# Performance work log

Measured on AMD Instinct MI355X. Metric: run time of the kernel, lower is better.

## Reference

```python
import jax, jax.numpy as jnp
import numpy as np
from jax import lax

B, LATENT, HC, COND_OUT, H, INPUT = 64, 512, 1024, 512, 1024, 389
S, SEQ = 16, 512
NOTES = SEQ // S  # 32 notes per subsequence
NL = 2


def _lstm_cell(x, h, c, Wih, Whh, bih, bhh):
    # PyTorch LSTM cell, gate order i, f, g, o
    g = x @ Wih.T + h @ Whh.T + bih + bhh
    i, f, gg, o = jnp.split(g, 4, axis=-1)
    c_new = jax.nn.sigmoid(f) * c + jax.nn.sigmoid(i) * jnp.tanh(gg)
    h_new = jax.nn.sigmoid(o) * jnp.tanh(c_new)
    return h_new, c_new


def setup_inputs() -> dict:
    key = jax.random.key(0)
    ks = iter(jax.random.split(key, 32))
    s = 0.03  # ~ PyTorch LSTM uniform(-1/sqrt(H), 1/sqrt(H)) scale
    def W(shape):
        return jax.random.normal(next(ks), shape, jnp.float32) * s
    return {
        "latent": jax.random.normal(next(ks), (B, LATENT), jnp.float32),
        "target": jax.random.randint(next(ks), (B, SEQ), 0, INPUT),
        "teacher_forcing": 0,
        "h0_dec": jax.random.normal(next(ks), (S, NL, B, H), jnp.float32),
        "c0_dec": jax.random.normal(next(ks), (S, NL, B, H), jnp.float32),
        # conductor LSTM (2 layers)
        "Wih_c0": W((4 * HC, LATENT)), "Whh_c0": W((4 * HC, HC)),
        "bih_c0": W((4 * HC,)), "bhh_c0": W((4 * HC,)),
        "Wih_c1": W((4 * HC, HC)), "Whh_c1": W((4 * HC, HC)),
        "bih_c1": W((4 * HC,)), "bhh_c1": W((4 * HC,)),
        # conductor output projection
        "Wco": W((COND_OUT, HC)), "bco": W((COND_OUT,)),
        # decoder LSTM (2 layers); input = concat(prev_note, emb) -> INPUT+COND_OUT
        "Wih_d0": W((4 * H, INPUT + COND_OUT)), "Whh_d0": W((4 * H, H)),
        "bih_d0": W((4 * H,)), "bhh_d0": W((4 * H,)),
        "Wih_d1": W((4 * H, H)), "Whh_d1": W((4 * H, H)),
        "bih_d1": W((4 * H,)), "bhh_d1": W((4 * H,)),
        # decoder output projection
        "Wdo": W((INPUT, H)), "bdo": W((INPUT,)),
    }


def reference(latent, target, teacher_forcing, h0_dec, c0_dec,
              Wih_c0, Whh_c0, bih_c0, bhh_c0, Wih_c1, Whh_c1, bih_c1, bhh_c1,
              Wco, bco,
              Wih_d0, Whh_d0, bih_d0, bhh_d0, Wih_d1, Whh_d1, bih_d1, bhh_d1,
              Wdo, bdo):
    # use_teacher_forcing is hard-coded False in the source; target is unused.
    del target, teacher_forcing

    def outer(carry, xs):
        hc, cc, prev = carry          # hc, cc: [2,B,HC]; prev: [B,INPUT]
        hd_init, cd_init = xs         # [2,B,H] random decoder init per subsequence
        h0, c0 = _lstm_cell(latent, hc[0], cc[0], Wih_c0, Whh_c0, bih_c0, bhh_c0)
        h1, c1 = _lstm_cell(h0, hc[1], cc[1], Wih_c1, Whh_c1, bih_c1, bhh_c1)
        emb = jnp.tanh(h1 @ Wco.T + bco)  # [B, COND_OUT]

        def inner(ic, _):
            p, hdi, cdi = ic
            x = jnp.concatenate([p, emb], axis=-1)  # [B, INPUT+COND_OUT]
            hd0, cd0 = _lstm_cell(x, hdi[0], cdi[0], Wih_d0, Whh_d0, bih_d0, bhh_d0)
            hd1, cd1 = _lstm_cell(hd0, hdi[1], cdi[1], Wih_d1, Whh_d1, bih_d1, bhh_d1)
            note = jnp.tanh(hd1 @ Wdo.T + bdo)  # [B, INPUT]
            return (note, jnp.stack([hd0, hd1]), jnp.stack([cd0, cd1])), note

        (prev_new, _, _), notes = lax.scan(inner, (prev, hd_init, cd_init), None, length=NOTES)
        return (jnp.stack([h0, h1]), jnp.stack([c0, c1]), prev_new), notes

    init = (jnp.zeros((NL, B, HC), jnp.float32),
            jnp.zeros((NL, B, HC), jnp.float32),
            jnp.zeros((B, INPUT), jnp.float32))
    _, out = lax.scan(outer, init, (h0_dec, c0_dec))
    # out: [S, NOTES, B, INPUT] -> [B, SEQ, INPUT]
    return out.transpose(2, 0, 1, 3).reshape(B, SEQ, INPUT)
```

## Files before the change

### kernel.cpp

```cpp
#include <hip/hip_runtime.h>
#include <hip/hip_bf16.h>

typedef unsigned int  u32;
typedef unsigned short u16;
typedef __attribute__((ext_vector_type(8))) short short8;
typedef __attribute__((ext_vector_type(4))) float f32x4;
typedef __attribute__((ext_vector_type(4))) unsigned int u32x4;
typedef __attribute__((ext_vector_type(2))) unsigned int u32x2;

#define MFMA(a,b,c) __builtin_amdgcn_mfma_f32_16x16x32_bf16(a,b,c,0,0,0)

#define NWG    256
#define KD0    1448
#define KD1    2056
#define KPROJ  1032

#define WS_ARR   0
#define WS_DONE  1024

#define WS_NOTE  4096
#define WS_HD0   (WS_NOTE + 2*52*64*8*2)
#define WS_HD1   (WS_HD0 + 2*128*64*8*2)
#define WS_HC0   (WS_HD1 + 2*128*64*8*2)
#define WS_HC1   (WS_HC0 + 2*128*64*8*2)
#define WS_EMB   (WS_HC1 + 2*128*64*8*2)
#define WS_LAT   (WS_EMB + 15*64*64*8*2)
#define WS_END   (WS_EMB + 16*64*64*8*2)

#define NOTE_PAR 26624
#define HD_PAR   65536
#define HC_PAR   65536
#define EMB_S    32768

#define L_GSC   0
#define L_GC0X  8448
#define L_CC0   12800
#define L_CC1   13824
#define L_BC1   14848
#define L_PACK  14912
#define L_ROLE  16960
#define L_WD0   L_ROLE
#define L_G0E   (L_ROLE + 32*KD0*2)
#define L_CST0  (L_G0E + 8448)
#define L_BD0   (L_CST0 + 2048)
#define L_WPJ   (L_BD0 + 128)
#define L_BPJ   (L_WPJ + 16*KPROJ*2)
#define L_WD1   L_ROLE
#define L_CST1  (L_ROLE + 32*KD1*2)
#define L_BD1   (L_CST1 + 2048)
#define LDS_BYTES 153600

__device__ __forceinline__ u16 f2bf(float f){
  u32 u = __float_as_uint(f);
  u32 r = (u + 0x7FFFu + ((u >> 16) & 1u)) >> 16;
  return (u16)r;
}
__device__ __forceinline__ float sigm(float x){ return 1.f/(1.f + __expf(-x)); }
__device__ __forceinline__ float tanh_(float x){
  float e = __expf(-2.f*fabsf(x));
  float t = (1.f - e)/(1.f + e);
  return x < 0.f ? -t : t;
}
__device__ __forceinline__ short8 ldw8(const float* p0){
  short8 r;
#pragma unroll
  for (int j = 0; j < 8; ++j) r[j] = (short)f2bf(p0[j]);
  return r;
}

__device__ __forceinline__ void gst1(u32* p, u32 v){
  asm volatile("global_store_dword %0, %1, off sc1" :: "v"(p), "v"(v) : "memory");
}
__device__ __forceinline__ void gst4(u16* p, u32x4 v){
  asm volatile("global_store_dwordx4 %0, %1, off sc1" :: "v"(p), "v"(v) : "memory");
}
__device__ __forceinline__ u32 ld1_sc1(const u32* p){
  u32 v;
  asm volatile("global_load_dword %0, %1, off sc1\n\ts_waitcnt vmcnt(0)"
               : "=v"(v) : "v"(p) : "memory");
  return v;
}

#define AISSUE(dst, addr) \
  asm volatile("global_load_dwordx4 %0, %1, off sc1" : "=&v"(dst) : "v"(addr) : "memory")
#define AWAITN(cnt) do{ \
  asm volatile("s_waitcnt vmcnt(" #cnt ")" ::: "memory"); \
  __builtin_amdgcn_sched_barrier(0x3F7); }while(0)

template<int NA, int NB, bool TWO>
__device__ __forceinline__ void mm_lds(
    const u16* Wl, int ldw16, const u16* xal, const u16* xbl,
    f32x4& a0, f32x4& a1)
{
  constexpr int N = NA + NB;
  short8 ab[(N < 16) ? N : 16];
#define XADDR(i) (((i) < NA) ? (xal + (size_t)(i)*2048) : (xbl + (size_t)((i)-NA)*2048))
#define ACONS(i) { \
    a0 = MFMA(ab[(i)&15], *(const short8*)(Wl + (size_t)(i)*32), a0); \
    if constexpr (TWO) a1 = MFMA(ab[(i)&15], *(const short8*)(Wl + ldw16 + (size_t)(i)*32), a1); }
  if constexpr (N <= 16){
#pragma unroll
    for (int i = 0; i < N; ++i) AISSUE(ab[i], XADDR(i));
    AWAITN(0);
#pragma unroll
    for (int i = 0; i < N; ++i) ACONS(i);
  } else {
#pragma unroll
    for (int i = 0; i < 16; ++i) AISSUE(ab[i], XADDR(i));
#pragma unroll
    for (int i = 0; i < N - 16; ++i){
      AWAITN(15);
      ACONS(i);
      AISSUE(ab[i & 15], XADDR(i + 16));
    }
#define ATAIL(j, c) AWAITN(c); ACONS(N - 16 + (j));
    ATAIL(0,15) ATAIL(1,14) ATAIL(2,13) ATAIL(3,12)
    ATAIL(4,11) ATAIL(5,10) ATAIL(6,9)  ATAIL(7,8)
    ATAIL(8,7)  ATAIL(9,6)  ATAIL(10,5) ATAIL(11,4)
    ATAIL(12,3) ATAIL(13,2) ATAIL(14,1) ATAIL(15,0)
#undef ATAIL
  }
#undef ACONS
#undef XADDR
}

template<int NA, int NB, bool TWO>
__device__ __forceinline__ void mm_gw(
    const float* w00, const float* w01, const float* w10, const float* w11,
    const u16* xal, const u16* xbl, f32x4& a0, f32x4& a1)
{
  constexpr int N = NA + NB;
  static_assert((N % 16) == 0, "");
  short8 ab[16];
#define XADDR(i) (((i) < NA) ? (xal + (size_t)(i)*2048) : (xbl + (size_t)((i)-NA)*2048))
#pragma unroll
  for (int b = 0; b < N/16; ++b){
#pragma unroll
    for (int j = 0; j < 16; ++j) AISSUE(ab[j], XADDR(b*16 + j));
    AWAITN(0);
#pragma unroll
    for (int j = 0; j < 16; ++j){
      const int i = b*16 + j;
      const float* wp0 = (i < NA) ? (w00 + (size_t)i*32) : (w01 + (size_t)(i-NA)*32);
      a0 = MFMA(ab[j], ldw8(wp0), a0);
      if constexpr (TWO){
        const float* wp1 = (i < NA) ? (w10 + (size_t)i*32) : (w11 + (size_t)(i-NA)*32);
        a1 = MFMA(ab[j], ldw8(wp1), a1);
      }
    }
  }
#undef XADDR
}

__device__ __forceinline__ void gbar(char* ws, int grp, int mem, u32 ep){
  u32* arr  = (u32*)(ws + WS_ARR) + grp*32;
  u32* done = (u32*)(ws + WS_DONE);
  asm volatile("s_waitcnt vmcnt(0)" ::: "memory");
  __syncthreads();
  if (threadIdx.x < 64){
    const int l = threadIdx.x;
    if (l == 0) gst1(&arr[mem], ep);
    if (mem == 0){
      for (;;){
        u32 m = (l < 32) ? ld1_sc1(&arr[l]) : ep;
#pragma unroll
        for (int off = 32; off; off >>= 1){
          u32 o = (u32)__shfl_xor((int)m, off, 64);
          m = o < m ? o : m;
        }
        if (m >= ep) break;
      }
      if (l == 0) gst1(&done[grp], ep);
    }
    for (;;){
      u32 m = (l < 8) ? ld1_sc1(&done[l]) : ep;
#pragma unroll
      for (int off = 32; off; off >>= 1){
        u32 o = (u32)__shfl_xor((int)m, off, 64);
        m = o < m ? o : m;
      }
      if (m >= ep) break;
      __builtin_amdgcn_s_sleep(1);
    }
  }
  __syncthreads();
}

struct Params {
  const float *latent, *h0_dec, *c0_dec;
  const float *Wih_c0, *Whh_c0, *bih_c0, *bhh_c0;
  const float *Wih_c1, *Whh_c1, *bih_c1, *bhh_c1;
  const float *Wco, *bco;
  const float *Wih_d0, *Whh_d0, *bih_d0, *bhh_d0;
  const float *Wih_d1, *Whh_d1, *bih_d1, *bhh_d1;
  const float *Wdo, *bdo;
  float* out;
  char* ws;
};

__device__ __forceinline__ void cell_pw(
    const float* g_sc, const float* gadd, const float* bias,
    float* cst, u32* pack, int tid)
{
  const int b = tid & 63, k = tid >> 6;
  u32 hp = 0;
#pragma unroll
  for (int j = 0; j < 2; ++j){
    const int u = 2*k + j;
    float gi = g_sc[b*33 + u];
    float gf = g_sc[b*33 + 8 + u];
    float gg = g_sc[b*33 + 16 + u];
    float go = g_sc[b*33 + 24 + u];
    if (gadd){
      gi += gadd[b*33 + u];      gf += gadd[b*33 + 8 + u];
      gg += gadd[b*33 + 16 + u]; go += gadd[b*33 + 24 + u];
    }
    if (bias){
      gi += bias[u]; gf += bias[8 + u]; gg += bias[16 + u]; go += bias[24 + u];
    }
    float c = sigm(gf)*cst[u*64 + b] + sigm(gi)*tanh_(gg);
    const float h = sigm(go)*tanh_(c);
    cst[u*64 + b] = c;
    hp |= ((u32)f2bf(h)) << (16*j);
  }
  pack[b*4 + k] = hp;
}

__device__ __forceinline__ void cond_pw(
    f32x4 acc, const float* gadd17, const float* bias16,
    float* cstL, u16* pack16, int lane, int wid)
{
  const int r = lane & 15, q = lane >> 4, m0 = wid*16;
  float v[4], vf[4], vg[4], vo[4];
#pragma unroll
  for (int i = 0; i < 4; ++i){
    const int brow = m0 + q*4 + i;
    float x = acc[i];
    if (gadd17) x += gadd17[brow*17 + r];
    if (bias16) x += bias16[r];
    v[i] = x;
  }
#pragma unroll
  for (int i = 0; i < 4; ++i){
    vf[i] = __shfl_xor(v[i], 4, 64);
    vg[i] = __shfl_xor(v[i], 8, 64);
    vo[i] = __shfl_xor(v[i], 12, 64);
  }
  if (r < 4){
#pragma unroll
    for (int i = 0; i < 4; ++i){
      const int brow = m0 + q*4 + i;
      float c = sigm(vf[i])*cstL[r*64 + brow] + sigm(v[i])*tanh_(vg[i]);
      const float h = sigm(vo[i])*tanh_(c);
      cstL[r*64 + brow] = c;
      pack16[brow*4 + r] = f2bf(h);
    }
  }
}

__global__ void init_kernel(const float* latent, char* ws){
  const int i = blockIdx.x*blockDim.x + threadIdx.x;
  if (i < 1024) ((u32*)ws)[i] = 0u;
  if (i < 26624) ((u32*)(ws + WS_NOTE))[i] = 0u;
  if (i < 65536){ ((u32*)(ws + WS_HC0))[i] = 0u; ((u32*)(ws + WS_HC1))[i] = 0u; }
  if (i < 32768){
    const int b = i >> 9, k = i & 511;
    ((u16*)(ws + WS_LAT))[((size_t)(k >> 3)*64 + b)*8 + (k & 7)] = f2bf(latent[i]);
  }
}

__global__ void __launch_bounds__(256, 1) decoder_kernel(Params P){
  extern __shared__ char smem[];
  const int wg = blockIdx.x, tid = threadIdx.x;
  const int lane = tid & 63, wid = tid >> 6;
  const int rr = lane & 15, q = lane >> 4, m0 = wid*16;
  const int grp = wg >> 5, mem = wg & 31;

  u16* noteb = (u16*)(P.ws + WS_NOTE);
  u16* hd0b  = (u16*)(P.ws + WS_HD0);
  u16* hd1b  = (u16*)(P.ws + WS_HD1);
  u16* hc0b  = (u16*)(P.ws + WS_HC0);
  u16* hc1b  = (u16*)(P.ws + WS_HC1);
  u16* embA  = (u16*)(P.ws + WS_EMB);
  const u16* latg = (const u16*)(P.ws + WS_LAT);

  float* g_sc  = (float*)(smem + L_GSC);
  float* g_c0x = (float*)(smem + L_GC0X);
  float* cc0   = (float*)(smem + L_CC0);
  float* cc1   = (float*)(smem + L_CC1);
  float* bc1   = (float*)(smem + L_BC1);
  u16*   pack16 = (u16*)(smem + L_PACK);
  u32*   packU32 = (u32*)(smem + L_PACK);
  u16*   Wd0  = (u16*)(smem + L_WD0);
  float* g0e  = (float*)(smem + L_G0E);
  float* cst0 = (float*)(smem + L_CST0);
  float* bd0  = (float*)(smem + L_BD0);
  u16*   Wpj  = (u16*)(smem + L_WPJ);
  float* bpj  = (float*)(smem + L_BPJ);
  u16*   Wd1  = (u16*)(smem + L_WD1);
  float* cst1 = (float*)(smem + L_CST1);
  float* bd1  = (float*)(smem + L_BD1);

  const bool is_d0 = (wg < 128);
  const int lofs = (q*64 + m0 + rr)*8;

  if (is_d0){
    for (int r = wid; r < 32; r += 4){
      const int grow = ((r >> 3) << 10) + 8*wg + (r & 7);
      const float* wih = P.Wih_d0 + (size_t)grow*901;
      const float* whh = P.Whh_d0 + (size_t)grow*1024;
      u16* dst = Wd0 + (size_t)r*KD0;
      for (int c = lane; c < 416; c += 64) dst[c] = (c < 389) ? f2bf(wih[c]) : (u16)0;
      for (int c = lane; c < 1024; c += 64) dst[416 + c] = f2bf(whh[c]);
    }
    if (tid < 32){
      const int grow = ((tid >> 3) << 10) + 8*wg + (tid & 7);
      bd0[tid] = P.bih_d0[grow] + P.bhh_d0[grow];
    }
    if (wg < 25){
      for (int r = wid; r < 16; r += 4){
        const int row = 16*wg + r;
        u16* dst = Wpj + (size_t)r*KPROJ;
        if (row < 389){
          const float* w = P.Wdo + (size_t)row*1024;
          for (int c = lane; c < 1024; c += 64) dst[c] = f2bf(w[c]);
        } else {
          for (int c = lane; c < 1024; c += 64) dst[c] = 0;
        }
      }
      if (tid < 16){
        const int row = 16*wg + tid;
        bpj[tid] = (row < 389) ? P.bdo[row] : 0.f;
      }
    }
  } else {
    const int wl = wg - 128;
    for (int r = wid; r < 32; r += 4){
      const int grow = ((r >> 3) << 10) + 8*wl + (r & 7);
      const float* wih = P.Wih_d1 + (size_t)grow*1024;
      const float* whh = P.Whh_d1 + (size_t)grow*1024;
      u16* dst = Wd1 + (size_t)r*KD1;
      for (int c = lane; c < 1024; c += 64) dst[c] = f2bf(wih[c]);
      for (int c = lane; c < 1024; c += 64) dst[1024 + c] = f2bf(whh[c]);
    }
    if (tid < 32){
      const int grow = ((tid >> 3) << 10) + 8*wl + (tid & 7);
      bd1[tid] = P.bih_d1[grow] + P.bhh_d1[grow];
    }
  }
  if (tid < 256){ cc0[tid] = 0.f; cc1[tid] = 0.f; }
  if (tid < 16){
    const int grow = ((tid >> 2) << 10) + 4*wg + (tid & 3);
    bc1[tid] = P.bih_c1[grow] + P.bhh_c1[grow];
  }
  {
    const int grow = ((rr >> 2) << 10) + 4*wg + (rr & 3);
    f32x4 acc = {0.f,0.f,0.f,0.f}, dummy;
    mm_gw<16,0,false>(P.Wih_c0 + (size_t)grow*512 + q*8, nullptr, nullptr, nullptr,
                      latg + lofs, latg + lofs, acc, dummy);
    const float bias = P.bih_c0[grow] + P.bhh_c0[grow];
#pragma unroll
    for (int i = 0; i < 4; ++i)
      g_c0x[(m0 + q*4 + i)*17 + rr] = acc[i] + bias;
  }
  __syncthreads();

  u32 ep = 0;
#define GBAR() gbar(P.ws, grp, mem, ++ep)

  for (int s = 0; s < 16; ++s){
    const int pc = s & 1;
    const u16* hc0_p = hc0b + (size_t)pc*HC_PAR;
    u16*       hc0_n = hc0b + (size_t)(pc ^ 1)*HC_PAR;
    const u16* hc1_p = hc1b + (size_t)pc*HC_PAR;
    u16*       hc1_n = hc1b + (size_t)(pc ^ 1)*HC_PAR;
    const int grow = ((rr >> 2) << 10) + 4*wg + (rr & 3);

    {
      f32x4 acc = {0.f,0.f,0.f,0.f}, dummy;
      mm_gw<32,0,false>(P.Whh_c0 + (size_t)grow*1024 + q*8, nullptr, nullptr, nullptr,
                        hc0_p + lofs, hc0_p + lofs, acc, dummy);
      cond_pw(acc, g_c0x, nullptr, cc0, pack16, lane, wid);
    }
    __syncthreads();
    if (tid < 64){
      u32x2 v = *(const u32x2*)&packU32[tid*2];
      asm volatile("global_store_dwordx2 %0, %1, off sc1"
                   :: "v"(hc0_n + ((size_t)(wg >> 1)*64 + tid)*8 + (wg & 1)*4), "v"(v) : "memory");
    }
    GBAR();

    {
      f32x4 acc = {0.f,0.f,0.f,0.f}, dummy;
      mm_gw<32,32,false>(P.Wih_c1 + (size_t)grow*1024 + q*8,
                         P.Whh_c1 + (size_t)grow*1024 + q*8, nullptr, nullptr,
                         hc0_n + lofs, hc1_p + lofs, acc, dummy);
      cond_pw(acc, nullptr, bc1, cc1, pack16, lane, wid);
    }
    __syncthreads();
    if (tid < 64){
      u32x2 v = *(const u32x2*)&packU32[tid*2];
      asm volatile("global_store_dwordx2 %0, %1, off sc1"
                   :: "v"(hc1_n + ((size_t)(wg >> 1)*64 + tid)*8 + (wg & 1)*4), "v"(v) : "memory");
    }
    GBAR();

    if (wg < 32){
      const int row = 16*wg + rr;
      f32x4 acc = {0.f,0.f,0.f,0.f}, dummy;
      mm_gw<32,0,false>(P.Wco + (size_t)row*1024 + q*8, nullptr, nullptr, nullptr,
                        hc1_n + lofs, hc1_n + lofs, acc, dummy);
      const float bias = P.bco[row];
#pragma unroll
      for (int i = 0; i < 4; ++i)
        pack16[(m0 + q*4 + i)*16 + rr] = f2bf(tanh_(acc[i] + bias));
      __syncthreads();
      if (tid < 64){
        u16* ea = embA + (size_t)s*EMB_S;
        u32x4 v0 = *(const u32x4*)&packU32[tid*8];
        u32x4 v1 = *(const u32x4*)&packU32[tid*8 + 4];
        gst4(ea + ((size_t)(2*wg)*64 + tid)*8, v0);
        gst4(ea + ((size_t)(2*wg + 1)*64 + tid)*8, v1);
      }
    }
    GBAR();
  }

  for (int s = 0; s < 16; ++s){
    f32x4 sh0 = {0.f,0.f,0.f,0.f}, sh1 = sh0;
    f32x4 t10 = sh0, t11 = sh0;

    if (is_d0){
      {
        const int b = tid & 63, k = tid >> 6;
        const size_t src = ((size_t)(s*2 + 0)*64 + b)*1024 + 8*wg + 2*k;
        cst0[(2*k)*64 + b]     = P.c0_dec[src];
        cst0[(2*k + 1)*64 + b] = P.c0_dec[src + 1];
        packU32[b*4 + k] = (u32)f2bf(P.h0_dec[src]) | ((u32)f2bf(P.h0_dec[src + 1]) << 16);
      }
      __syncthreads();
      if (tid < 64){
        u32x4 v = *(const u32x4*)&packU32[tid*4];
        gst4(hd0b + ((size_t)wg*64 + tid)*8, v);
      }
      {
        const int g0 = ((rr >> 3) << 10) + 8*wg + (rr & 7);
        const int g1 = (((rr + 16) >> 3) << 10) + 8*wg + (rr & 7);
        f32x4 a0 = {0.f,0.f,0.f,0.f}, a1 = {0.f,0.f,0.f,0.f};
        const u16* ea = embA + (size_t)s*EMB_S;
        mm_gw<16,0,true>(P.Wih_d0 + (size_t)g0*901 + 389 + q*8, nullptr,
                         P.Wih_d0 + (size_t)g1*901 + 389 + q*8, nullptr,
                         ea + lofs, ea + lofs, a0, a1);
#pragma unroll
        for (int i = 0; i < 4; ++i){
          g0e[(m0 + q*4 + i)*33 + rr]      = a0[i] + bd0[rr];
          g0e[(m0 + q*4 + i)*33 + 16 + rr] = a1[i] + bd0[rr + 16];
        }
      }
    } else {
      const int wl = wg - 128;
      const int b = tid & 63, k = tid >> 6;
      const size_t src = ((size_t)(s*2 + 1)*64 + b)*1024 + 8*wl + 2*k;
      cst1[(2*k)*64 + b]     = P.c0_dec[src];
      cst1[(2*k + 1)*64 + b] = P.c0_dec[src + 1];
      packU32[b*4 + k] = (u32)f2bf(P.h0_dec[src]) | ((u32)f2bf(P.h0_dec[src + 1]) << 16);
      __syncthreads();
      if (tid < 64){
        u32x4 v = *(const u32x4*)&packU32[tid*4];
        gst4(hd1b + ((size_t)wl*64 + tid)*8, v);
      }
    }
    GBAR();

    for (int t = 0; t < 32; ++t){
      const int p = t & 1;
      const u16* note_p = noteb + (size_t)p*NOTE_PAR;
      u16*       note_n = noteb + (size_t)(p ^ 1)*NOTE_PAR;
      const u16* hd0_p = hd0b + (size_t)p*HD_PAR;
      u16*       hd0_n = hd0b + (size_t)(p ^ 1)*HD_PAR;
      const u16* hd1_p = hd1b + (size_t)p*HD_PAR;
      u16*       hd1_n = hd1b + (size_t)(p ^ 1)*HD_PAR;

      if (is_d0){
        f32x4 a0, a1;
        if (t == 0){
          a0 = (f32x4){0.f,0.f,0.f,0.f}; a1 = a0;
          mm_lds<13,32,true>(Wd0 + (size_t)rr*KD0 + q*8, 16*KD0,
                             note_p + lofs, hd0_p + lofs, a0, a1);
        } else {
          a0 = sh0; a1 = sh1;
          mm_lds<13,0,true>(Wd0 + (size_t)rr*KD0 + q*8, 16*KD0,
                            note_p + lofs, note_p + lofs, a0, a1);
        }
#pragma unroll
        for (int i = 0; i < 4; ++i){
          g_sc[(m0 + q*4 + i)*33 + rr]      = a0[i];
          g_sc[(m0 + q*4 + i)*33 + 16 + rr] = a1[i];
        }
        __syncthreads();
        cell_pw(g_sc, g0e, nullptr, cst0, packU32, tid);
        __syncthreads();
        if (tid < 64){
          u32x4 v = *(const u32x4*)&packU32[tid*4];
          gst4(hd0_n + ((size_t)wg*64 + tid)*8, v);
        }
      }
      GBAR();

      if (!is_d0){
        f32x4 a0, a1;
        if (t == 0){
          a0 = (f32x4){0.f,0.f,0.f,0.f}; a1 = a0;
          mm_lds<32,32,true>(Wd1 + (size_t)rr*KD1 + q*8, 16*KD1,
                             hd0_n + lofs, hd1_p + lofs, a0, a1);
        } else {
          a0 = t10; a1 = t11;
          mm_lds<32,0,true>(Wd1 + (size_t)rr*KD1 + q*8, 16*KD1,
                            hd0_n + lofs, hd0_n + lofs, a0, a1);
        }
#pragma unroll
        for (int i = 0; i < 4; ++i){
          g_sc[(m0 + q*4 + i)*33 + rr]      = a0[i];
          g_sc[(m0 + q*4 + i)*33 + 16 + rr] = a1[i];
        }
        __syncthreads();
        cell_pw(g_sc, nullptr, bd1, cst1, packU32, tid);
        __syncthreads();
        if (tid < 64){
          u32x4 v = *(const u32x4*)&packU32[tid*4];
          gst4(hd1_n + ((size_t)(wg - 128)*64 + tid)*8, v);
        }
      } else {
        sh0 = (f32x4){0.f,0.f,0.f,0.f}; sh1 = sh0;
        mm_lds<32,0,true>(Wd0 + (size_t)rr*KD0 + 416 + q*8, 16*KD0,
                          hd0_n + lofs, hd0_n + lofs, sh0, sh1);
      }
      GBAR();

      if (wg < 25){
        f32x4 a0 = {0.f,0.f,0.f,0.f}, a1;
        mm_lds<32,0,false>(Wpj + (size_t)rr*KPROJ + q*8, 0,
                           hd1_n + lofs, hd1_n + lofs, a0, a1);
        const int row = 16*wg + rr;
        const int seq = s*32 + t;
        const float bias = bpj[rr];
#pragma unroll
        for (int i = 0; i < 4; ++i){
          const int brow = m0 + q*4 + i;
          const float nv = tanh_(a0[i] + bias);
          if (row < 389) P.out[((size_t)brow*512 + seq)*389 + row] = nv;
          pack16[brow*16 + rr] = f2bf(nv);
        }
        __syncthreads();
        if (tid < 64){
          u32x4 v0 = *(const u32x4*)&packU32[tid*8];
          u32x4 v1 = *(const u32x4*)&packU32[tid*8 + 4];
          gst4(note_n + ((size_t)(2*wg)*64 + tid)*8, v0);
          gst4(note_n + ((size_t)(2*wg + 1)*64 + tid)*8, v1);
        }
      }
      if (!is_d0){
        t10 = (f32x4){0.f,0.f,0.f,0.f}; t11 = t10;
        mm_lds<32,0,true>(Wd1 + (size_t)rr*KD1 + 1024 + q*8, 16*KD1,
                          hd1_n + lofs, hd1_n + lofs, t10, t11);
      }
      GBAR();
    }
  }
#undef GBAR
}

extern "C" void kernel_launch(void* const* d_in, const int* in_sizes, int n_in,
                              void* d_out, int out_size, void* d_ws, size_t ws_size,
                              hipStream_t stream){
  (void)in_sizes; (void)n_in; (void)out_size;
  if (ws_size < (size_t)WS_END) return;

  Params P;
  P.latent = (const float*)d_in[0];
  P.h0_dec = (const float*)d_in[3];
  P.c0_dec = (const float*)d_in[4];
  P.Wih_c0 = (const float*)d_in[5];  P.Whh_c0 = (const float*)d_in[6];
  P.bih_c0 = (const float*)d_in[7];  P.bhh_c0 = (const float*)d_in[8];
  P.Wih_c1 = (const float*)d_in[9];  P.Whh_c1 = (const float*)d_in[10];
  P.bih_c1 = (const float*)d_in[11]; P.bhh_c1 = (const float*)d_in[12];
  P.Wco    = (const float*)d_in[13]; P.bco    = (const float*)d_in[14];
  P.Wih_d0 = (const float*)d_in[15]; P.Whh_d0 = (const float*)d_in[16];
  P.bih_d0 = (const float*)d_in[17]; P.bhh_d0 = (const float*)d_in[18];
  P.Wih_d1 = (const float*)d_in[19]; P.Whh_d1 = (const float*)d_in[20];
  P.bih_d1 = (const float*)d_in[21]; P.bhh_d1 = (const float*)d_in[22];
  P.Wdo    = (const float*)d_in[23]; P.bdo    = (const float*)d_in[24];
  P.out = (float*)d_out;
  P.ws  = (char*)d_ws;

  hipLaunchKernelGGL(init_kernel, dim3(256), dim3(256), 0, stream,
                     (const float*)d_in[0], (char*)d_ws);

  hipFuncSetAttribute(reinterpret_cast<const void*>(&decoder_kernel),
                      hipFuncAttributeMaxDynamicSharedMemorySize, LDS_BYTES);
  hipLaunchKernelGGL(decoder_kernel, dim3(NWG), dim3(256), LDS_BYTES, stream, P);
}
```

Before: 9.247 ms.

## Replace decoder-loop global barriers with per-stage counting semaphores

Drops the three grid-wide barriers per decoder step. Each dependency now uses its own monotonically increasing counter (hd0, hd1, note, init), so layer-0, layer-1 and projection workgroups wait only for the data they actually consume. The recurrent-term matmuls are also skipped on the last step of each subsequence, where their results are never used. The aim is to cut barrier latency and let the stages overlap. The cost is more complex ordering logic, which relies on the counters starting at zero and on the double-buffer reuse still being safe.

```diff
diff --git a/kernel.cpp b/kernel.cpp
--- a/kernel.cpp
+++ b/kernel.cpp
@@ -17,6 +17,12 @@
 
 #define WS_ARR   0
 #define WS_DONE  1024
+#define WS_SEM   1536
+#define SEM_HD0  0
+#define SEM_HD1  1
+#define SEM_NOTE 2
+#define SEM_I0   3
+#define SEM_I1   4
 
 #define WS_NOTE  4096
 #define WS_HD0   (WS_NOTE + 2*52*64*8*2)
@@ -152,6 +158,30 @@
 #undef XADDR
 }
 
+__device__ __forceinline__ void sem_post(char* ws, int sem, int wg){
+  asm volatile("s_waitcnt vmcnt(0)" ::: "memory");
+  __syncthreads();
+  if (threadIdx.x == 0){
+    u32* c = (u32*)(ws + WS_SEM + sem*512 + (wg & 7)*64);
+    __hip_atomic_fetch_add(c, 1u, __ATOMIC_RELAXED, __HIP_MEMORY_SCOPE_AGENT);
+  }
+}
+__device__ __forceinline__ void sem_wait(char* ws, int sem, u32 target, bool slp){
+  if (threadIdx.x < 64){
+    const int l = threadIdx.x;
+    const u32* c = (const u32*)(ws + WS_SEM + sem*512 + l*64);
+    for (;;){
+      u32 v = (l < 8) ? ld1_sc1(c) : 0u;
+#pragma unroll
+      for (int off = 32; off; off >>= 1)
+        v += (u32)__shfl_xor((int)v, off, 64);
+      if (v >= target) break;
+      if (slp) __builtin_amdgcn_s_sleep(1);
+    }
+  }
+  __syncthreads();
+}
+
 __device__ __forceinline__ void gbar(char* ws, int grp, int mem, u32 ep){
   u32* arr  = (u32*)(ws + WS_ARR) + grp*32;
   u32* done = (u32*)(ws + WS_DONE);
@@ -427,8 +457,11 @@
   }
 
   for (int s = 0; s < 16; ++s){
+    const u32 n0 = (u32)s*32u;
     f32x4 sh0 = {0.f,0.f,0.f,0.f}, sh1 = sh0;
     f32x4 t10 = sh0, t11 = sh0;
+
+    sem_wait(P.ws, SEM_NOTE, 25u*n0, true);
 
     if (is_d0){
       {
@@ -443,6 +476,7 @@
         u32x4 v = *(const u32x4*)&packU32[tid*4];
         gst4(hd0b + ((size_t)wg*64 + tid)*8, v);
       }
+      sem_post(P.ws, SEM_I0, wg);
       {
         const int g0 = ((rr >> 3) << 10) + 8*wg + (rr & 7);
         const int g1 = (((rr + 16) >> 3) << 10) + 8*wg + (rr & 7);
@@ -457,6 +491,7 @@
           g0e[(m0 + q*4 + i)*33 + 16 + rr] = a1[i] + bd0[rr + 16];
         }
       }
+      __syncthreads();
     } else {
       const int wl = wg - 128;
       const int b = tid & 63, k = tid >> 6;
@@ -469,10 +504,11 @@
         u32x4 v = *(const u32x4*)&packU32[tid*4];
         gst4(hd1b + ((size_t)wl*64 + tid)*8, v);
       }
-    }
-    GBAR();
+      sem_post(P.ws, SEM_I1, wg);
+    }
 
     for (int t = 0; t < 32; ++t){
+      const u32 n = n0 + (u32)t;
       const int p = t & 1;
       const u16* note_p = noteb + (size_t)p*NOTE_PAR;
       u16*       note_n = noteb + (size_t)(p ^ 1)*NOTE_PAR;
@@ -482,6 +518,9 @@
       u16*       hd1_n = hd1b + (size_t)(p ^ 1)*HD_PAR;
 
       if (is_d0){
+        if (t == 0) sem_wait(P.ws, SEM_I0, 128u*(u32)(s + 1), false);
+        else        sem_wait(P.ws, SEM_NOTE, 25u*n, false);
+
         f32x4 a0, a1;
         if (t == 0){
           a0 = (f32x4){0.f,0.f,0.f,0.f}; a1 = a0;
@@ -504,10 +543,43 @@
           u32x4 v = *(const u32x4*)&packU32[tid*4];
           gst4(hd0_n + ((size_t)wg*64 + tid)*8, v);
         }
-      }
-      GBAR();
-
-      if (!is_d0){
+        sem_post(P.ws, SEM_HD0, wg);
+
+        if (t < 31){
+          sem_wait(P.ws, SEM_HD0, 128u*(n + 1u), false);
+          sh0 = (f32x4){0.f,0.f,0.f,0.f}; sh1 = sh0;
+          mm_lds<32,0,true>(Wd0 + (size_t)rr*KD0 + 416 + q*8, 16*KD0,
+                            hd0_n + lofs, hd0_n + lofs, sh0, sh1);
+        }
+
+        if (wg < 25){
+          sem_wait(P.ws, SEM_HD1, 128u*(n + 1u), false);
+          f32x4 b0 = {0.f,0.f,0.f,0.f}, b1;
+          mm_lds<32,0,false>(Wpj + (size_t)rr*KPROJ + q*8, 0,
+                             hd1_n + lofs, hd1_n + lofs, b0, b1);
+          const int row = 16*wg + rr;
+          const int seq = s*32 + t;
+          const float bias = bpj[rr];
+#pragma unroll
+          for (int i = 0; i < 4; ++i){
+            const int brow = m0 + q*4 + i;
+            const float nv = tanh_(b0[i] + bias);
+            if (row < 389) P.out[((size_t)brow*512 + seq)*389 + row] = nv;
+            pack16[brow*16 + rr] = f2bf(nv);
+          }
+          __syncthreads();
+          if (tid < 64){
+            u32x4 v0 = *(const u32x4*)&packU32[tid*8];
+            u32x4 v1 = *(const u32x4*)&packU32[tid*8 + 4];
+            gst4(note_n + ((size_t)(2*wg)*64 + tid)*8, v0);
+            gst4(note_n + ((size_t)(2*wg + 1)*64 + tid)*8, v1);
+          }
+          sem_post(P.ws, SEM_NOTE, wg);
+        }
+      } else {
+        sem_wait(P.ws, SEM_HD0, 128u*(n + 1u), false);
+        if (t == 0) sem_wait(P.ws, SEM_I1, 128u*(u32)(s + 1), false);
+
         f32x4 a0, a1;
         if (t == 0){
           a0 = (f32x4){0.f,0.f,0.f,0.f}; a1 = a0;
@@ -530,41 +602,15 @@
           u32x4 v = *(const u32x4*)&packU32[tid*4];
           gst4(hd1_n + ((size_t)(wg - 128)*64 + tid)*8, v);
         }
-      } else {
-        sh0 = (f32x4){0.f,0.f,0.f,0.f}; sh1 = sh0;
-        mm_lds<32,0,true>(Wd0 + (size_t)rr*KD0 + 416 + q*8, 16*KD0,
-                          hd0_n + lofs, hd0_n + lofs, sh0, sh1);
-      }
-      GBAR();
-
-      if (wg < 25){
-        f32x4 a0 = {0.f,0.f,0.f,0.f}, a1;
-        mm_lds<32,0,false>(Wpj + (size_t)rr*KPROJ + q*8, 0,
-                           hd1_n + lofs, hd1_n + lofs, a0, a1);
-        const int row = 16*wg + rr;
-        const int seq = s*32 + t;
-        const float bias = bpj[rr];
-#pragma unroll
-        for (int i = 0; i < 4; ++i){
-          const int brow = m0 + q*4 + i;
-          const float nv = tanh_(a0[i] + bias);
-          if (row < 389) P.out[((size_t)brow*512 + seq)*389 + row] = nv;
-          pack16[brow*16 + rr] = f2bf(nv);
-        }
-        __syncthreads();
-        if (tid < 64){
-          u32x4 v0 = *(const u32x4*)&packU32[tid*8];
-          u32x4 v1 = *(const u32x4*)&packU32[tid*8 + 4];
-          gst4(note_n + ((size_t)(2*wg)*64 + tid)*8, v0);
-          gst4(note_n + ((size_t)(2*wg + 1)*64 + tid)*8, v1);
-        }
-      }
-      if (!is_d0){
-        t10 = (f32x4){0.f,0.f,0.f,0.f}; t11 = t10;
-        mm_lds<32,0,true>(Wd1 + (size_t)rr*KD1 + 1024 + q*8, 16*KD1,
-                          hd1_n + lofs, hd1_n + lofs, t10, t11);
-      }
-      GBAR();
+        sem_post(P.ws, SEM_HD1, wg);
+
+        if (t < 31){
+          sem_wait(P.ws, SEM_HD1, 128u*(n + 1u), false);
+          t10 = (f32x4){0.f,0.f,0.f,0.f}; t11 = t10;
+          mm_lds<32,0,true>(Wd1 + (size_t)rr*KD1 + 1024 + q*8, 16*KD1,
+                            hd1_n + lofs, hd1_n + lofs, t10, t11);
+        }
+      }
     }
   }
 #undef GBAR
```

Measured after the change: 9.346 ms. Within noise of the previous version (+1.1%).
